# Optimization experiments

Measured on AMD Instinct MI355X. Metric: run time of the kernel, lower is better.

Reference implementation:

```python
import jax, jax.numpy as jnp
import numpy as np

DIM = 1024
HEADS = 16
HEAD_DIM = DIM // HEADS

def setup_inputs() -> dict:
    key = jax.random.key(0)
    ks = jax.random.split(key, 6)
    s = 0.02
    return {
        "x": jax.random.normal(ks[0], (2, 2048, DIM), dtype=jnp.float32),
        "w_qkv": jax.random.normal(ks[1], (DIM, 3 * DIM), dtype=jnp.float32) * s,
        "w_proj": jax.random.normal(ks[2], (DIM, DIM), dtype=jnp.float32) * s,
        "b_proj": jnp.zeros((DIM,), dtype=jnp.float32),
        "ln_gamma": jnp.ones((DIM,), dtype=jnp.float32),
        "ln_beta": jnp.zeros((DIM,), dtype=jnp.float32),
    }

def layer_norm(x, gamma, beta, eps=1e-5):
    mu = jnp.mean(x, axis=-1, keepdims=True)
    var = jnp.var(x, axis=-1, keepdims=True)
    return (x - mu) * jax.lax.rsqrt(var + eps) * gamma + beta

def reference(x, w_qkv, w_proj, b_proj, ln_gamma, ln_beta):
    B, N, C = x.shape
    residual = x
    h = layer_norm(x, ln_gamma, ln_beta)
    qkv = h @ w_qkv  # [B,N,3C]
    qkv = qkv.reshape(B, N, 3, HEADS, HEAD_DIM)
    q = jnp.transpose(qkv[:, :, 0], (0, 2, 1, 3))  # [B,H,N,D]
    k = jnp.transpose(qkv[:, :, 1], (0, 2, 1, 3))
    v = jnp.transpose(qkv[:, :, 2], (0, 2, 1, 3))
    scale = 1.0 / jnp.sqrt(jnp.float32(HEAD_DIM))
    attn = jnp.einsum('bhqd,bhkd->bhqk', q, k) * scale
    attn = jax.nn.softmax(attn, axis=-1)
    out = jnp.einsum('bhqk,bhkd->bhqd', attn, v)  # [B,H,N,D]
    out = jnp.transpose(out, (0, 2, 1, 3)).reshape(B, N, C)
    out = out @ w_proj + b_proj
    return out + residual
```

## Files before the change

kernel.cpp:

```cpp
#include <hip/hip_runtime.h>

#define DIM   1024
#define HEADS 16
#define HDIM  64
#define BATCH 2
#define SEQ   2048
#define TOK   (BATCH*SEQ)
#define MEG   1048576

typedef __bf16 bf16x8 __attribute__((ext_vector_type(8)));
typedef float  f32x4  __attribute__((ext_vector_type(4)));

__device__ __forceinline__ float b2f(ushort u) {
    union { unsigned int u32; float f; } x; x.u32 = ((unsigned int)u) << 16; return x.f;
}
__device__ __forceinline__ ushort f2b(float f) {
    union { float f; unsigned int u32; } x; x.f = f;
    unsigned int r = x.u32 + 0x7FFFu + ((x.u32 >> 16) & 1u);
    return (ushort)(r >> 16);
}
__device__ __forceinline__ unsigned int pack2bf(float a, float b) {
    union { float f; unsigned int u; } xa, xb; xa.f = a; xb.f = b;
    return (xb.u & 0xFFFF0000u) | (xa.u >> 16);
}
__device__ __forceinline__ void gload_lds16(const ushort* g, void* l) {
    __builtin_amdgcn_global_load_lds((const __attribute__((address_space(1))) void*)g,
                                     (__attribute__((address_space(3))) void*)l, 16, 0, 0);
}

__global__ void transpose_f2b_k(const float* __restrict__ src, ushort* __restrict__ dst,
                                int R, int Cc) {
    __shared__ ushort tile[32][33];
    int c0 = blockIdx.x * 32, r0 = blockIdx.y * 32;
    int tx = threadIdx.x, ty = threadIdx.y;
#pragma unroll
    for (int i = 0; i < 4; i++)
        tile[ty + 8 * i][tx] = f2b(src[(long)(r0 + ty + 8 * i) * Cc + c0 + tx]);
    __syncthreads();
#pragma unroll
    for (int i = 0; i < 4; i++)
        dst[(long)(c0 + ty + 8 * i) * R + r0 + tx] = tile[tx][ty + 8 * i];
}

__global__ void transpose_bf16_k(const ushort* __restrict__ src, ushort* __restrict__ dst,
                                 int R, int Cc, long sstride, long dstride) {
    __shared__ ushort tile[32][33];
    long b = blockIdx.z;
    const ushort* s = src + b * sstride;
    ushort* d = dst + b * dstride;
    int c0 = blockIdx.x * 32, r0 = blockIdx.y * 32;
    int tx = threadIdx.x, ty = threadIdx.y;
#pragma unroll
    for (int i = 0; i < 4; i++)
        tile[ty + 8 * i][tx] = s[(long)(r0 + ty + 8 * i) * Cc + c0 + tx];
    __syncthreads();
#pragma unroll
    for (int i = 0; i < 4; i++)
        d[(long)(c0 + ty + 8 * i) * R + r0 + tx] = tile[tx][ty + 8 * i];
}

__global__ __launch_bounds__(256)
void ln_k(const float* __restrict__ x, const float* __restrict__ gamma,
          const float* __restrict__ beta, ushort* __restrict__ h) {
    __shared__ float red[8];
    int row = blockIdx.x, tid = threadIdx.x;
    const float* xr = x + (long)row * DIM;
    float4 xv = *(const float4*)(xr + tid * 4);
    float s1 = xv.x + xv.y + xv.z + xv.w;
    float s2 = xv.x * xv.x + xv.y * xv.y + xv.z * xv.z + xv.w * xv.w;
#pragma unroll
    for (int off = 32; off; off >>= 1) {
        s1 += __shfl_down(s1, off);
        s2 += __shfl_down(s2, off);
    }
    int wid = tid >> 6, lane = tid & 63;
    if (lane == 0) { red[wid * 2] = s1; red[wid * 2 + 1] = s2; }
    __syncthreads();
    s1 = red[0] + red[2] + red[4] + red[6];
    s2 = red[1] + red[3] + red[5] + red[7];
    float mu  = s1 * (1.0f / DIM);
    float var = s2 * (1.0f / DIM) - mu * mu;
    float rs  = rsqrtf(var + 1e-5f);
    float4 gv = *(const float4*)(gamma + tid * 4);
    float4 bv = *(const float4*)(beta + tid * 4);
    ushort4 ov;
    ov.x = f2b((xv.x - mu) * rs * gv.x + bv.x);
    ov.y = f2b((xv.y - mu) * rs * gv.y + bv.y);
    ov.z = f2b((xv.z - mu) * rs * gv.z + bv.z);
    ov.w = f2b((xv.w - mu) * rs * gv.w + bv.w);
    *(ushort4*)(h + (long)row * DIM + tid * 4) = ov;
}

__global__ __launch_bounds__(256, 3)
void gemm_qkv_k(const ushort* __restrict__ A, const ushort* __restrict__ Bt,
                ushort* __restrict__ qp, ushort* __restrict__ kp, ushort* __restrict__ vp) {
    __shared__ ushort As[2][128][32];
    __shared__ ushort Bs[2][128][32];
    int tid  = threadIdx.x;
    int wid  = tid >> 6, lane = tid & 63;
    int quad = lane >> 4, l16 = lane & 15;
    int wm = wid >> 1, wn = wid & 1;
    int rowbase = blockIdx.y * 128;
    int colbase = blockIdx.x * 128;
    int arow = lane >> 2;
    int acol = (lane & 3) * 8;

    f32x4 acc[4][4];
#pragma unroll
    for (int i = 0; i < 4; i++)
#pragma unroll
        for (int j = 0; j < 4; j++) acc[i][j] = (f32x4){0.f, 0.f, 0.f, 0.f};

    for (int k0 = 0; k0 < DIM; k0 += 64) {
#pragma unroll
        for (int p = 0; p < 2; p++) {
            int c = wid * 2 + p;
            int r = c * 16 + arow;
#pragma unroll
            for (int pnl = 0; pnl < 2; pnl++) {
                int cc = k0 + pnl * 32 + acol;
                gload_lds16(A  + (long)(rowbase + r) * DIM + cc, &As[pnl][c * 16][0]);
                gload_lds16(Bt + (long)(colbase + r) * DIM + cc, &Bs[pnl][c * 16][0]);
            }
        }
        __syncthreads();
#pragma unroll
        for (int pnl = 0; pnl < 2; pnl++) {
            bf16x8 fa[4], fb[4];
#pragma unroll
            for (int t = 0; t < 4; t++)
                fa[t] = *(const bf16x8*)(&As[pnl][wm * 64 + t * 16 + l16][quad * 8]);
#pragma unroll
            for (int t = 0; t < 4; t++)
                fb[t] = *(const bf16x8*)(&Bs[pnl][wn * 64 + t * 16 + l16][quad * 8]);
#pragma unroll
            for (int i = 0; i < 4; i++)
#pragma unroll
                for (int j = 0; j < 4; j++)
                    acc[i][j] = __builtin_amdgcn_mfma_f32_16x16x32_bf16(fa[i], fb[j], acc[i][j], 0, 0, 0);
        }
        __syncthreads();
    }

#pragma unroll
    for (int i = 0; i < 4; i++)
#pragma unroll
        for (int j = 0; j < 4; j++) {
            int m0  = rowbase + wm * 64 + i * 16 + quad * 4;
            int col = colbase + wn * 64 + j * 16 + l16;
            int part = col >> 10, rem = col & 1023;
            int head = rem >> 6, d = rem & 63;
            ushort* dst = (part == 0) ? qp : (part == 1) ? kp : vp;
#pragma unroll
            for (int r = 0; r < 4; r++) {
                float v = acc[i][j][r];
                int mm = m0 + r;
                int b = mm >> 11, nn = mm & 2047;
                float sv = (part == 0) ? v * 0.125f : v;
                dst[((((long)b * HEADS + head) * SEQ + nn) << 6) + d] = f2b(sv);
            }
        }
}

__global__ __launch_bounds__(256, 3)
void gemm_proj_k(const ushort* __restrict__ A, const ushort* __restrict__ Bt,
                 const float* __restrict__ bias, const float* __restrict__ xres,
                 float* __restrict__ outp) {
    __shared__ ushort As[2][128][32];
    __shared__ ushort Bs[2][64][32];
    int tid  = threadIdx.x;
    int wid  = tid >> 6, lane = tid & 63;
    int quad = lane >> 4, l16 = lane & 15;
    int rowbase = blockIdx.y * 128;
    int colbase = blockIdx.x * 64;
    int arow = lane >> 2, acol = (lane & 3) * 8;

    f32x4 acc[2][4];
#pragma unroll
    for (int i = 0; i < 2; i++)
#pragma unroll
        for (int j = 0; j < 4; j++) acc[i][j] = (f32x4){0.f, 0.f, 0.f, 0.f};

    for (int k0 = 0; k0 < DIM; k0 += 64) {
#pragma unroll
        for (int p = 0; p < 2; p++) {
            int c = wid * 2 + p;
            int r = c * 16 + arow;
            int mm = rowbase + r;
            int bq = mm >> 11, nn = mm & 2047;
#pragma unroll
            for (int pnl = 0; pnl < 2; pnl++) {
                int cc = k0 + pnl * 32 + acol;
                int head = cc >> 6, d = cc & 63;
                gload_lds16(A + ((((long)bq * HEADS + head) * SEQ + nn) << 6) + d,
                            &As[pnl][c * 16][0]);
            }
        }
        {
            int r = wid * 16 + arow;
#pragma unroll
            for (int pnl = 0; pnl < 2; pnl++) {
                int cc = k0 + pnl * 32 + acol;
                gload_lds16(Bt + (long)(colbase + r) * DIM + cc, &Bs[pnl][wid * 16][0]);
            }
        }
        __syncthreads();
#pragma unroll
        for (int pnl = 0; pnl < 2; pnl++) {
            bf16x8 fa[2], fb[4];
#pragma unroll
            for (int t = 0; t < 2; t++)
                fa[t] = *(const bf16x8*)(&As[pnl][wid * 32 + t * 16 + l16][quad * 8]);
#pragma unroll
            for (int t = 0; t < 4; t++)
                fb[t] = *(const bf16x8*)(&Bs[pnl][t * 16 + l16][quad * 8]);
#pragma unroll
            for (int i = 0; i < 2; i++)
#pragma unroll
                for (int j = 0; j < 4; j++)
                    acc[i][j] = __builtin_amdgcn_mfma_f32_16x16x32_bf16(fa[i], fb[j], acc[i][j], 0, 0, 0);
        }
        __syncthreads();
    }

#pragma unroll
    for (int i = 0; i < 2; i++)
#pragma unroll
        for (int j = 0; j < 4; j++) {
            int m0  = rowbase + wid * 32 + i * 16 + quad * 4;
            int col = colbase + j * 16 + l16;
#pragma unroll
            for (int r = 0; r < 4; r++) {
                int mm = m0 + r;
                outp[(long)mm * DIM + col] = acc[i][j][r] + bias[col] + xres[(long)mm * DIM + col];
            }
        }
}

__global__ __launch_bounds__(256, 2)
void attn_k(ushort* qio, const ushort* __restrict__ k,
            const ushort* __restrict__ vt) {
    __shared__ ushort Kp[2][2][1312];
    __shared__ ushort Vs[2][64][40];
    __shared__ ushort plds[4][2][16][40];
    int bh = blockIdx.y;
    int tid = threadIdx.x, wid = tid >> 6, lane = tid & 63;
    int quad = lane >> 4, l16 = lane & 15;
    ushort* qh = qio + (long)bh * SEQ * HDIM;
    const ushort* kh = k  + (long)bh * SEQ * HDIM;
    const ushort* vh = vt + (long)bh * HDIM * SEQ;

    int krow = tid >> 3, kc8 = (tid & 7) * 8;
    int kpan = kc8 >> 5, kcp = kc8 & 31;
    int koff = krow * 40 + kcp;
    int vrow = tid >> 2, vcol = (tid & 3) * 8;

    int qrow0 = blockIdx.x * 128 + wid * 32;
    bf16x8 qf[2][2];
#pragma unroll
    for (int s = 0; s < 2; s++) {
        qf[s][0] = *(const bf16x8*)(qh + (long)(qrow0 + s * 16 + l16) * HDIM + quad * 8);
        qf[s][1] = *(const bf16x8*)(qh + (long)(qrow0 + s * 16 + l16) * HDIM + 32 + quad * 8);
    }

    f32x4 o[2][4];
    f32x4 lac[2][2];
#pragma unroll
    for (int s = 0; s < 2; s++) {
#pragma unroll
        for (int dc = 0; dc < 4; dc++) o[s][dc] = (f32x4){0.f, 0.f, 0.f, 0.f};
        lac[s][0] = (f32x4){0.f, 0.f, 0.f, 0.f};
        lac[s][1] = (f32x4){0.f, 0.f, 0.f, 0.f};
    }

    uint4 kreg = *(const uint4*)(kh + (long)krow * HDIM + kc8);
    uint4 vreg = *(const uint4*)(vh + (long)vrow * SEQ + vcol);
    *(uint4*)(&Kp[0][kpan][koff]) = kreg;
    *(uint4*)(&Vs[0][vrow][vcol]) = vreg;

    const int NIT = SEQ / 32;
    for (int it = 0; it < NIT; ++it) {
        int buf = it & 1;
        if (it + 1 < NIT) {
            int kt = (it + 1) * 32;
            kreg = *(const uint4*)(kh + (long)(kt + krow) * HDIM + kc8);
            vreg = *(const uint4*)(vh + (long)vrow * SEQ + kt + vcol);
        }
        __syncthreads();

        bf16x8 kb[2][2];
#pragma unroll
        for (int t = 0; t < 2; t++)
#pragma unroll
            for (int p = 0; p < 2; p++)
                kb[t][p] = *(const bf16x8*)(&Kp[buf][p][(t * 16 + l16) * 40 + quad * 8]);

        f32x4 sc[2][2];
#pragma unroll
        for (int s = 0; s < 2; s++)
#pragma unroll
            for (int t = 0; t < 2; t++) {
                f32x4 z = (f32x4){0.f, 0.f, 0.f, 0.f};
                z = __builtin_amdgcn_mfma_f32_16x16x32_bf16(kb[t][0], qf[s][0], z, 0, 0, 0);
                z = __builtin_amdgcn_mfma_f32_16x16x32_bf16(kb[t][1], qf[s][1], z, 0, 0, 0);
                sc[s][t] = z;
            }

#pragma unroll
        for (int s = 0; s < 2; s++)
#pragma unroll
            for (int t = 0; t < 2; t++) {
                float e0 = __expf(sc[s][t][0]);
                float e1 = __expf(sc[s][t][1]);
                float e2 = __expf(sc[s][t][2]);
                float e3 = __expf(sc[s][t][3]);
                lac[s][t] += (f32x4){e0, e1, e2, e3};
                uint2 pk;
                pk.x = pack2bf(e0, e1);
                pk.y = pack2bf(e2, e3);
                *(uint2*)(&plds[wid][s][l16][t * 16 + quad * 4]) = pk;
            }
        asm volatile("s_waitcnt lgkmcnt(0)" ::: "memory");

        bf16x8 pf[2];
#pragma unroll
        for (int s = 0; s < 2; s++)
            pf[s] = *(const bf16x8*)(&plds[wid][s][l16][quad * 8]);
#pragma unroll
        for (int dc = 0; dc < 4; dc++) {
            bf16x8 vfb = *(const bf16x8*)(&Vs[buf][dc * 16 + l16][quad * 8]);
#pragma unroll
            for (int s = 0; s < 2; s++)
                o[s][dc] = __builtin_amdgcn_mfma_f32_16x16x32_bf16(pf[s], vfb, o[s][dc], 0, 0, 0);
        }

        if (it + 1 < NIT) {
            *(uint4*)(&Kp[buf ^ 1][kpan][koff]) = kreg;
            *(uint4*)(&Vs[buf ^ 1][vrow][vcol]) = vreg;
        }
    }

#pragma unroll
    for (int s = 0; s < 2; s++) {
        f32x4 lv = lac[s][0] + lac[s][1];
        float t = lv[0] + lv[1] + lv[2] + lv[3];
        t += __shfl_xor(t, 16);
        t += __shfl_xor(t, 32);
        float linv_q = 1.0f / t;
        float linv[4];
#pragma unroll
        for (int r = 0; r < 4; r++)
            linv[r] = __shfl(linv_q, quad * 4 + r);
        int rowo = qrow0 + s * 16 + quad * 4;
#pragma unroll
        for (int dc = 0; dc < 4; dc++)
#pragma unroll
            for (int r = 0; r < 4; r++)
                qh[(long)(rowo + r) * HDIM + dc * 16 + l16] = f2b(o[s][dc][r] * linv[r]);
    }
}

extern "C" void kernel_launch(void* const* d_in, const int* in_sizes, int n_in,
                              void* d_out, int out_size, void* d_ws, size_t ws_size,
                              hipStream_t stream) {
    const float* x      = (const float*)d_in[0];
    const float* w_qkv  = (const float*)d_in[1];
    const float* w_proj = (const float*)d_in[2];
    const float* b_proj = (const float*)d_in[3];
    const float* gamma  = (const float*)d_in[4];
    const float* beta   = (const float*)d_in[5];
    float* out = (float*)d_out;

    ushort* ws   = (ushort*)d_ws;
    ushort* h_vt = ws;
    ushort* wqt  = ws + (size_t)4 * MEG;
    ushort* qb   = ws + (size_t)7 * MEG;
    ushort* kb   = ws + (size_t)11 * MEG;
    ushort* vb   = ws + (size_t)15 * MEG;

    transpose_f2b_k<<<dim3(3 * DIM / 32, DIM / 32), dim3(32, 8), 0, stream>>>(
        w_qkv, wqt, DIM, 3 * DIM);
    ln_k<<<dim3(TOK), dim3(256), 0, stream>>>(x, gamma, beta, h_vt);
    gemm_qkv_k<<<dim3(3 * DIM / 128, TOK / 128), dim3(256), 0, stream>>>(
        h_vt, wqt, qb, kb, vb);
    transpose_bf16_k<<<dim3(HDIM / 32, SEQ / 32, BATCH * HEADS), dim3(32, 8), 0, stream>>>(
        vb, h_vt, SEQ, HDIM, (long)SEQ * HDIM, (long)SEQ * HDIM);
    attn_k<<<dim3(SEQ / 128, BATCH * HEADS), dim3(256), 0, stream>>>(qb, kb, h_vt);
    transpose_f2b_k<<<dim3(DIM / 32, DIM / 32), dim3(32, 8), 0, stream>>>(
        w_proj, kb, DIM, DIM);
    gemm_proj_k<<<dim3(DIM / 64, TOK / 128), dim3(256), 0, stream>>>(
        qb, kb, b_proj, x, out);
}
```

Baseline: 201.0 us.

## Fuse V transpose into QKV GEMM epilogue and repad attention LDS tiles

The QKV GEMM now writes V directly in transposed [B,H,D,N] layout by staging the output tile through shared memory, which removes the separate bf16 transpose kernel and its extra round trip through global memory. The attention kernel's K, V and P shared-memory tiles switch to a row stride of 72 elements with different thread-to-element load mappings, aiming to reduce LDS bank conflicts. The trade-offs are more LDS per attention block, which may limit occupancy, plus a divergent epilogue and an extra barrier in the GEMM for V tiles.

```diff
diff --git a/kernel.cpp b/kernel.cpp
--- a/kernel.cpp
+++ b/kernel.cpp
@@ -40,23 +40,6 @@
 #pragma unroll
     for (int i = 0; i < 4; i++)
         dst[(long)(c0 + ty + 8 * i) * R + r0 + tx] = tile[tx][ty + 8 * i];
-}
-
-__global__ void transpose_bf16_k(const ushort* __restrict__ src, ushort* __restrict__ dst,
-                                 int R, int Cc, long sstride, long dstride) {
-    __shared__ ushort tile[32][33];
-    long b = blockIdx.z;
-    const ushort* s = src + b * sstride;
-    ushort* d = dst + b * dstride;
-    int c0 = blockIdx.x * 32, r0 = blockIdx.y * 32;
-    int tx = threadIdx.x, ty = threadIdx.y;
-#pragma unroll
-    for (int i = 0; i < 4; i++)
-        tile[ty + 8 * i][tx] = s[(long)(r0 + ty + 8 * i) * Cc + c0 + tx];
-    __syncthreads();
-#pragma unroll
-    for (int i = 0; i < 4; i++)
-        d[(long)(c0 + ty + 8 * i) * R + r0 + tx] = tile[tx][ty + 8 * i];
 }
 
 __global__ __launch_bounds__(256)
@@ -94,16 +77,13 @@
 __global__ __launch_bounds__(256, 3)
 void gemm_qkv_k(const ushort* __restrict__ A, const ushort* __restrict__ Bt,
                 ushort* __restrict__ qp, ushort* __restrict__ kp, ushort* __restrict__ vp) {
-    __shared__ ushort As[2][128][32];
-    __shared__ ushort Bs[2][128][32];
+    __shared__ ushort smem[16384];
     int tid  = threadIdx.x;
     int wid  = tid >> 6, lane = tid & 63;
     int quad = lane >> 4, l16 = lane & 15;
     int wm = wid >> 1, wn = wid & 1;
     int rowbase = blockIdx.y * 128;
     int colbase = blockIdx.x * 128;
-    int arow = lane >> 2;
-    int acol = (lane & 3) * 8;
 
     f32x4 acc[4][4];
 #pragma unroll
@@ -115,12 +95,15 @@
 #pragma unroll
         for (int p = 0; p < 2; p++) {
             int c = wid * 2 + p;
-            int r = c * 16 + arow;
+            int r = c * 16 + (lane >> 2);
+            int ac = (lane & 3) * 8;
 #pragma unroll
             for (int pnl = 0; pnl < 2; pnl++) {
-                int cc = k0 + pnl * 32 + acol;
-                gload_lds16(A  + (long)(rowbase + r) * DIM + cc, &As[pnl][c * 16][0]);
-                gload_lds16(Bt + (long)(colbase + r) * DIM + cc, &Bs[pnl][c * 16][0]);
+                int cc = k0 + pnl * 32 + ac;
+                gload_lds16(A  + (long)(rowbase + r) * DIM + cc,
+                            &smem[pnl * 4096 + c * 16 * 32]);
+                gload_lds16(Bt + (long)(colbase + r) * DIM + cc,
+                            &smem[8192 + pnl * 4096 + c * 16 * 32]);
             }
         }
         __syncthreads();
@@ -129,10 +112,10 @@
             bf16x8 fa[4], fb[4];
 #pragma unroll
             for (int t = 0; t < 4; t++)
-                fa[t] = *(const bf16x8*)(&As[pnl][wm * 64 + t * 16 + l16][quad * 8]);
+                fa[t] = *(const bf16x8*)(&smem[pnl * 4096 + (wm * 64 + t * 16 + l16) * 32 + quad * 8]);
 #pragma unroll
             for (int t = 0; t < 4; t++)
-                fb[t] = *(const bf16x8*)(&Bs[pnl][wn * 64 + t * 16 + l16][quad * 8]);
+                fb[t] = *(const bf16x8*)(&smem[8192 + pnl * 4096 + (wn * 64 + t * 16 + l16) * 32 + quad * 8]);
 #pragma unroll
             for (int i = 0; i < 4; i++)
 #pragma unroll
@@ -142,24 +125,49 @@
         __syncthreads();
     }
 
-#pragma unroll
-    for (int i = 0; i < 4; i++)
-#pragma unroll
-        for (int j = 0; j < 4; j++) {
-            int m0  = rowbase + wm * 64 + i * 16 + quad * 4;
-            int col = colbase + wn * 64 + j * 16 + l16;
-            int part = col >> 10, rem = col & 1023;
-            int head = rem >> 6, d = rem & 63;
-            ushort* dst = (part == 0) ? qp : (part == 1) ? kp : vp;
-#pragma unroll
-            for (int r = 0; r < 4; r++) {
-                float v = acc[i][j][r];
-                int mm = m0 + r;
-                int b = mm >> 11, nn = mm & 2047;
-                float sv = (part == 0) ? v * 0.125f : v;
-                dst[((((long)b * HEADS + head) * SEQ + nn) << 6) + d] = f2b(sv);
-            }
-        }
+    if (colbase >= 2048) {
+#pragma unroll
+        for (int i = 0; i < 4; i++)
+#pragma unroll
+            for (int j = 0; j < 4; j++) {
+                int cl = wn * 64 + j * 16 + l16;
+                int rl = wm * 64 + i * 16 + quad * 4;
+#pragma unroll
+                for (int r = 0; r < 4; r++)
+                    smem[cl * 128 + rl + r] = f2b(acc[i][j][r]);
+            }
+        __syncthreads();
+        int b = rowbase >> 11, nnb = rowbase & 2047;
+        int hbase = (colbase - 2048) >> 6;
+#pragma unroll
+        for (int i = 0; i < 8; i++) {
+            int id = i * 256 + tid;
+            int cl = id >> 4;
+            int off = (id & 15) * 8;
+            int hh = hbase + (cl >> 6), d = cl & 63;
+            uint4 val = *(const uint4*)(&smem[cl * 128 + off]);
+            *(uint4*)(vp + (((long)b * HEADS + hh) * HDIM + d) * SEQ + nnb + off) = val;
+        }
+    } else {
+#pragma unroll
+        for (int i = 0; i < 4; i++)
+#pragma unroll
+            for (int j = 0; j < 4; j++) {
+                int m0  = rowbase + wm * 64 + i * 16 + quad * 4;
+                int col = colbase + wn * 64 + j * 16 + l16;
+                int part = col >> 10, rem = col & 1023;
+                int head = rem >> 6, d = rem & 63;
+                ushort* dst = (part == 0) ? qp : kp;
+#pragma unroll
+                for (int r = 0; r < 4; r++) {
+                    float v = acc[i][j][r];
+                    int mm = m0 + r;
+                    int b = mm >> 11, nn = mm & 2047;
+                    float sv = (part == 0) ? v * 0.125f : v;
+                    dst[((((long)b * HEADS + head) * SEQ + nn) << 6) + d] = f2b(sv);
+                }
+            }
+    }
 }
 
 __global__ __launch_bounds__(256, 3)
@@ -240,9 +248,9 @@
 __global__ __launch_bounds__(256, 2)
 void attn_k(ushort* qio, const ushort* __restrict__ k,
             const ushort* __restrict__ vt) {
-    __shared__ ushort Kp[2][2][1312];
-    __shared__ ushort Vs[2][64][40];
-    __shared__ ushort plds[4][2][16][40];
+    __shared__ ushort Kp[2][2][2304];
+    __shared__ ushort Vs[2][4608];
+    __shared__ ushort plds[4][2][1152];
     int bh = blockIdx.y;
     int tid = threadIdx.x, wid = tid >> 6, lane = tid & 63;
     int quad = lane >> 4, l16 = lane & 15;
@@ -250,10 +258,11 @@
     const ushort* kh = k  + (long)bh * SEQ * HDIM;
     const ushort* vh = vt + (long)bh * HDIM * SEQ;
 
-    int krow = tid >> 3, kc8 = (tid & 7) * 8;
+    int krow = tid & 31, kc8 = (tid >> 5) * 8;
     int kpan = kc8 >> 5, kcp = kc8 & 31;
-    int koff = krow * 40 + kcp;
-    int vrow = tid >> 2, vcol = (tid & 3) * 8;
+    int koff = krow * 72 + kcp;
+    int vrow = tid & 63, vcol = (tid >> 6) * 8;
+    int voff = vrow * 72 + vcol;
 
     int qrow0 = blockIdx.x * 128 + wid * 32;
     bf16x8 qf[2][2];
@@ -276,7 +285,7 @@
     uint4 kreg = *(const uint4*)(kh + (long)krow * HDIM + kc8);
     uint4 vreg = *(const uint4*)(vh + (long)vrow * SEQ + vcol);
     *(uint4*)(&Kp[0][kpan][koff]) = kreg;
-    *(uint4*)(&Vs[0][vrow][vcol]) = vreg;
+    *(uint4*)(&Vs[0][voff]) = vreg;
 
     const int NIT = SEQ / 32;
     for (int it = 0; it < NIT; ++it) {
@@ -293,7 +302,7 @@
         for (int t = 0; t < 2; t++)
 #pragma unroll
             for (int p = 0; p < 2; p++)
-                kb[t][p] = *(const bf16x8*)(&Kp[buf][p][(t * 16 + l16) * 40 + quad * 8]);
+                kb[t][p] = *(const bf16x8*)(&Kp[buf][p][(t * 16 + l16) * 72 + quad * 8]);
 
         f32x4 sc[2][2];
 #pragma unroll
@@ -318,17 +327,17 @@
                 uint2 pk;
                 pk.x = pack2bf(e0, e1);
                 pk.y = pack2bf(e2, e3);
-                *(uint2*)(&plds[wid][s][l16][t * 16 + quad * 4]) = pk;
+                *(uint2*)(&plds[wid][s][l16 * 72 + t * 16 + quad * 4]) = pk;
             }
         asm volatile("s_waitcnt lgkmcnt(0)" ::: "memory");
 
         bf16x8 pf[2];
 #pragma unroll
         for (int s = 0; s < 2; s++)
-            pf[s] = *(const bf16x8*)(&plds[wid][s][l16][quad * 8]);
+            pf[s] = *(const bf16x8*)(&plds[wid][s][l16 * 72 + quad * 8]);
 #pragma unroll
         for (int dc = 0; dc < 4; dc++) {
-            bf16x8 vfb = *(const bf16x8*)(&Vs[buf][dc * 16 + l16][quad * 8]);
+            bf16x8 vfb = *(const bf16x8*)(&Vs[buf][(dc * 16 + l16) * 72 + quad * 8]);
 #pragma unroll
             for (int s = 0; s < 2; s++)
                 o[s][dc] = __builtin_amdgcn_mfma_f32_16x16x32_bf16(pf[s], vfb, o[s][dc], 0, 0, 0);
@@ -336,7 +345,7 @@
 
         if (it + 1 < NIT) {
             *(uint4*)(&Kp[buf ^ 1][kpan][koff]) = kreg;
-            *(uint4*)(&Vs[buf ^ 1][vrow][vcol]) = vreg;
+            *(uint4*)(&Vs[buf ^ 1][voff]) = vreg;
         }
     }
 
@@ -372,20 +381,18 @@
     float* out = (float*)d_out;
 
     ushort* ws   = (ushort*)d_ws;
-    ushort* h_vt = ws;
+    ushort* h    = ws;
     ushort* wqt  = ws + (size_t)4 * MEG;
     ushort* qb   = ws + (size_t)7 * MEG;
     ushort* kb   = ws + (size_t)11 * MEG;
-    ushort* vb   = ws + (size_t)15 * MEG;
+    ushort* vtb  = ws + (size_t)15 * MEG;
 
     transpose_f2b_k<<<dim3(3 * DIM / 32, DIM / 32), dim3(32, 8), 0, stream>>>(
         w_qkv, wqt, DIM, 3 * DIM);
-    ln_k<<<dim3(TOK), dim3(256), 0, stream>>>(x, gamma, beta, h_vt);
+    ln_k<<<dim3(TOK), dim3(256), 0, stream>>>(x, gamma, beta, h);
     gemm_qkv_k<<<dim3(3 * DIM / 128, TOK / 128), dim3(256), 0, stream>>>(
-        h_vt, wqt, qb, kb, vb);
-    transpose_bf16_k<<<dim3(HDIM / 32, SEQ / 32, BATCH * HEADS), dim3(32, 8), 0, stream>>>(
-        vb, h_vt, SEQ, HDIM, (long)SEQ * HDIM, (long)SEQ * HDIM);
-    attn_k<<<dim3(SEQ / 128, BATCH * HEADS), dim3(256), 0, stream>>>(qb, kb, h_vt);
+        h, wqt, qb, kb, vtb);
+    attn_k<<<dim3(SEQ / 128, BATCH * HEADS), dim3(256), 0, stream>>>(qb, kb, vtb);
     transpose_f2b_k<<<dim3(DIM / 32, DIM / 32), dim3(32, 8), 0, stream>>>(
         w_proj, kb, DIM, DIM);
     gemm_proj_k<<<dim3(DIM / 64, TOK / 128), dim3(256), 0, stream>>>(
```

Result: faster. 191.6 us (-4.7%).
